# Kernel optimization log

Hardware: AMD Instinct MI355X
Metric: run time of the kernel (lower is better)

Reference implementation:

```python
import jax, jax.numpy as jnp
import numpy as np

B, F, D = 16384, 256, 128
H = [512, 256]
OUT = 8
VOCAB = 100000


def setup_inputs() -> dict:
    key = jax.random.key(0)
    ks = jax.random.split(key, 16)
    s = lambda k, *sh: jax.random.normal(k, sh, jnp.float32) * 0.05
    return dict(
        features=jax.random.normal(ks[0], (B, F), jnp.float32),
        ent_idx=jax.random.randint(ks[1], (B,), 0, VOCAB),
        target=jax.random.randint(ks[2], (B,), 0, OUT),
        Wf=s(ks[3], F, D), bf=jnp.zeros((D,), jnp.float32),
        Wu=s(ks[4], D, D), bu=jnp.zeros((D,), jnp.float32),
        w_cf=s(ks[5], D), w_fc=s(ks[6], D),
        w_ef=s(ks[7], D), w_fe=s(ks[8], D),
        b_c=jnp.zeros((1,), jnp.float32), b_e=jnp.zeros((1,), jnp.float32),
        head_tab=s(ks[9], VOCAB, D), ent_tab=s(ks[10], VOCAB, D),
        W0=s(ks[11], 2 * D, H[0]), b0=jnp.zeros((H[0],), jnp.float32),
        W1=s(ks[12], H[0], H[1]), b1=jnp.zeros((H[1],), jnp.float32),
        W2=s(ks[13], H[1], OUT), b2=jnp.zeros((OUT,), jnp.float32),
    )


def cross_compress(f, e, w_cf, w_fc, w_ef, w_fe, b_c, b_e):
    # torch code builds c = f (outer) e of shape (B,D,D) then matmuls a (D,1)
    # vector; algebraically (f e^T) w = f * (e . w), so we use the O(B*D) form.
    ew_cf = e @ w_cf  # (B,)
    fw_fc = f @ w_fc
    ew_ef = e @ w_ef
    fw_fe = f @ w_fe
    new_f = f * ew_cf[:, None] + e * fw_fc[:, None] + b_c
    new_e = f * ew_ef[:, None] + e * fw_fe[:, None] + b_e
    return new_f, new_e


def reference(features, ent_idx, target, Wf, bf, Wu, bu, w_cf, w_fc, w_ef,
              w_fe, b_c, b_e, head_tab, ent_tab, W0, b0, W1, b1, W2, b2):
    # 'rec' branch of CompanyOperationEvaluation.forward (eval mode, dropout=id)
    cf = jax.nn.relu(features @ Wf + bf)          # feature_layer
    e = ent_tab[ent_idx]                           # entity_embed lookup
    h = head_tab[ent_idx]                          # head_embed lookup (same ids)
    for _ in range(2):
        cf = jax.nn.relu(cf @ Wu + bu)             # user_low_mlp_layer
        h, e = cross_compress(h, e, w_cf, w_fc, w_ef, w_fe, b_c, b_e)
    high = jnp.concatenate([cf, e], axis=1)        # (B, 2D)
    x = jax.nn.relu(high @ W0 + b0)
    x = jax.nn.relu(x @ W1 + b1)
    x = jax.nn.relu(x @ W2 + b2)                   # pred_last_layer
    prob = jax.nn.softmax(x, axis=1)
    return (prob, target)
```

## Files before the change

kernel.cpp:

```cpp
#include <hip/hip_runtime.h>
#include <hip/hip_bf16.h>


typedef __bf16 bf16x8 __attribute__((ext_vector_type(8)));
typedef float floatx4 __attribute__((ext_vector_type(4)));

__device__ __forceinline__ unsigned short f2bf(float x) {
  unsigned int u = __builtin_bit_cast(unsigned int, x);
  u = (u + 0x7FFFu + ((u >> 16) & 1u)) >> 16;
  return (unsigned short)u;
}

__device__ __forceinline__ int sz(int row, int col) {
  return col ^ ((row & 7) << 3);
}

#define PHASE_BAR()                                                  \
  do {                                                               \
    asm volatile("s_waitcnt vmcnt(0) lgkmcnt(0)" ::: "memory");      \
    __builtin_amdgcn_s_barrier();                                    \
    __builtin_amdgcn_sched_barrier(0);                               \
  } while (0)

__global__ __launch_bounds__(256) void prep_kernel(
    const float* __restrict__ Wf, const float* __restrict__ Wu,
    const float* __restrict__ W0, const float* __restrict__ W1,
    const float* __restrict__ W2,
    unsigned short* __restrict__ wfT, unsigned short* __restrict__ wuT,
    unsigned short* __restrict__ w0T, unsigned short* __restrict__ w1T,
    unsigned short* __restrict__ w2T) {
  __shared__ unsigned short tile[32][34];
  const int bid = blockIdx.x, tid = threadIdx.x;
  if (bid < 304) {
    int t = bid;
    const float* src; unsigned short* dst; int N, K, kt, nt;
    if (t < 32)       { src = Wf; dst = wfT; N = 128; K = 256; kt = t >> 2;       nt = t & 3; }
    else if (t < 48)  { t -= 32;  src = Wu; dst = wuT; N = 128; K = 128; kt = t >> 2; nt = t & 3; }
    else if (t < 176) { t -= 48;  src = W0; dst = w0T; N = 512; K = 256; kt = t >> 4; nt = t & 15; }
    else              { t -= 176; src = W1; dst = w1T; N = 256; K = 512; kt = t >> 3; nt = t & 7; }
    {
      int r = tid >> 3, cg = (tid & 7) * 4;
      float4 v = *(const float4*)(src + (size_t)(kt * 32 + r) * N + nt * 32 + cg);
      tile[r][cg + 0] = f2bf(v.x); tile[r][cg + 1] = f2bf(v.y);
      tile[r][cg + 2] = f2bf(v.z); tile[r][cg + 3] = f2bf(v.w);
    }
    __syncthreads();
    {
      int rp = tid >> 3, cg = (tid & 7) * 4;
      uint2 o;
      o.x = (unsigned)tile[cg + 0][rp] | ((unsigned)tile[cg + 1][rp] << 16);
      o.y = (unsigned)tile[cg + 2][rp] | ((unsigned)tile[cg + 3][rp] << 16);
      *(uint2*)(dst + (size_t)(nt * 32 + rp) * K + kt * 32 + cg) = o;
    }
  } else {
#pragma unroll
    for (int i = 0; i < 8; ++i) {
      int g = tid * 8 + i, k = g >> 3, n = g & 7;
      w2T[n * 256 + k] = f2bf(W2[g]);
    }
  }
}

template <int LDK>
__device__ __forceinline__ void stageB(unsigned short* dstbase,
                                       const unsigned short* __restrict__ src,
                                       int tid) {
#pragma unroll
  for (int i = 0; i < 4; ++i) {
    int chunk = i * 256 + tid;
    int row = chunk >> 3, segs = chunk & 7;
    int segl = segs ^ (row & 7);
    const unsigned short* g = src + (size_t)row * LDK + segl * 8;
    unsigned short* d = dstbase + chunk * 8;
    __builtin_amdgcn_global_load_lds((const unsigned int*)g, (unsigned int*)d,
                                     16, 0, 0);
  }
}

template <int PASS_STEPS, int LDK>
__device__ __forceinline__ const unsigned short* srcstep(
    const unsigned short* __restrict__ s, int st) {
  return s + (size_t)(st / PASS_STEPS) * 128 * LDK + (st % PASS_STEPS) * 64;
}

template <int LDA>
__device__ __forceinline__ void mstep(const unsigned short* A,
                                      const unsigned short* bt, int k0,
                                      floatx4* acc, int m16, int quad,
                                      int wave) {
#pragma unroll
  for (int kk = 0; kk < 64; kk += 32) {
    const int ca = k0 + kk + quad * 8;
    const int cb = kk + quad * 8;
    const int ra0 = m16, ra1 = 16 + m16;
    const int rb0 = wave * 32 + m16, rb1 = wave * 32 + 16 + m16;
    bf16x8 a0 = *(const bf16x8*)&A[ra0 * LDA + sz(ra0, ca)];
    bf16x8 a1 = *(const bf16x8*)&A[ra1 * LDA + sz(ra1, ca)];
    bf16x8 b0 = *(const bf16x8*)&bt[rb0 * 64 + sz(rb0, cb)];
    bf16x8 b1 = *(const bf16x8*)&bt[rb1 * 64 + sz(rb1, cb)];
    acc[0] = __builtin_amdgcn_mfma_f32_16x16x32_bf16(a0, b0, acc[0], 0, 0, 0);
    acc[1] = __builtin_amdgcn_mfma_f32_16x16x32_bf16(a0, b1, acc[1], 0, 0, 0);
    acc[2] = __builtin_amdgcn_mfma_f32_16x16x32_bf16(a1, b0, acc[2], 0, 0, 0);
    acc[3] = __builtin_amdgcn_mfma_f32_16x16x32_bf16(a1, b1, acc[3], 0, 0, 0);
  }
}

template <int T, int LDA, int PASS_STEPS, int LDK>
__device__ __forceinline__ void gemm_phase(
    const unsigned short* A, const unsigned short* __restrict__ src,
    unsigned short* b_sh, floatx4* acc, int tid, int m16, int quad, int wave) {
  stageB<LDK>(b_sh, srcstep<PASS_STEPS, LDK>(src, 0), tid);
  PHASE_BAR();
#pragma unroll
  for (int t = 0; t < T; ++t) {
    if (t + 1 < T)
      stageB<LDK>(b_sh + ((t + 1) & 1) * 8192,
                  srcstep<PASS_STEPS, LDK>(src, t + 1), tid);
    mstep<LDA>(A, b_sh + (t & 1) * 8192, (t % PASS_STEPS) * 64,
               acc + (t / PASS_STEPS) * 4, m16, quad, wave);
    PHASE_BAR();
  }
}

__global__ __launch_bounds__(256, 2) void fused_mlp_kernel(
    const float* __restrict__ features, const int* __restrict__ ent_idx,
    const float* __restrict__ head_tab, const float* __restrict__ ent_tab,
    const float* __restrict__ w_cf, const float* __restrict__ w_fc,
    const float* __restrict__ w_ef, const float* __restrict__ w_fe,
    const float* __restrict__ b_c, const float* __restrict__ b_e,
    const unsigned short* __restrict__ wfT,
    const unsigned short* __restrict__ wuT, const float* __restrict__ bf_,
    const float* __restrict__ bu,
    const unsigned short* __restrict__ w0T, const float* __restrict__ b0,
    const unsigned short* __restrict__ w1T, const float* __restrict__ b1,
    const unsigned short* __restrict__ w2T, const float* __restrict__ b2,
    const int* __restrict__ target, float* __restrict__ out) {
  __shared__ __align__(16) unsigned short regionA[16384];
  __shared__ __align__(16) unsigned short b_sh[2 * 8192];
  __shared__ __align__(16) unsigned short w2_sh[2048];
  __shared__ __align__(16) float cw_sh[512];
  unsigned short* feat_sh = regionA;
  unsigned short* buf0 = regionA + 8192;
  unsigned short* buf1 = regionA + 12288;
  unsigned short* A_sh = regionA;
  unsigned short* x0_sh = regionA;
  unsigned short* x1_sh = b_sh;

  const int tid = threadIdx.x;
  const int r0 = blockIdx.x * 32;
  const int lane = tid & 63, wave = tid >> 6;
  const int m16 = lane & 15, quad = lane >> 4;

  const int grow = tid >> 3, gpart = tid & 7;
  const int gidx = ent_idx[r0 + grow];
  const float* hp = head_tab + (size_t)gidx * 128 + gpart * 16;
  const float* ep = ent_tab + (size_t)gidx * 128 + gpart * 16;
  float4 h4[4], e4[4];
#pragma unroll
  for (int j = 0; j < 4; ++j) {
    h4[j] = *(const float4*)(hp + j * 4);
    e4[j] = *(const float4*)(ep + j * 4);
  }
  if (tid < 128) {
    int a = tid >> 5, o = (tid & 31) * 4;
    const float* s = (a == 0) ? w_cf : (a == 1) ? w_fc : (a == 2) ? w_ef : w_fe;
    *(float4*)&cw_sh[a * 128 + o] = *(const float4*)(s + o);
  }
  *(uint4*)&w2_sh[tid * 8] = *(const uint4*)(w2T + tid * 8);

#pragma unroll
  for (int i = 0; i < 8; ++i) {
    int idx4 = i * 256 + tid;
    int row = idx4 >> 6, c = (idx4 & 63) * 4;
    float4 v = *(const float4*)(features + (size_t)(r0 + row) * 256 + c);
    uint2 o;
    o.x = (unsigned)f2bf(v.x) | ((unsigned)f2bf(v.y) << 16);
    o.y = (unsigned)f2bf(v.z) | ((unsigned)f2bf(v.w) << 16);
    *(uint2*)&feat_sh[row * 256 + sz(row, c)] = o;
  }

  floatx4 acc[4];
#pragma unroll
  for (int j = 0; j < 4; ++j) acc[j] = (floatx4){0.f, 0.f, 0.f, 0.f};
  gemm_phase<4, 256, 4, 256>(feat_sh, wfT, b_sh, acc, tid, m16, quad, wave);
#pragma unroll
  for (int mi = 0; mi < 2; ++mi)
#pragma unroll
    for (int ni = 0; ni < 2; ++ni) {
      int col = wave * 32 + ni * 16 + m16;
      float bv = bf_[col];
#pragma unroll
      for (int r = 0; r < 4; ++r) {
        int row = mi * 16 + quad * 4 + r;
        buf0[row * 128 + sz(row, col)] =
            f2bf(fmaxf(acc[mi * 2 + ni][r] + bv, 0.f));
      }
    }

  {
    float h[16], e[16];
#pragma unroll
    for (int j = 0; j < 4; ++j) {
      h[4 * j + 0] = h4[j].x; h[4 * j + 1] = h4[j].y;
      h[4 * j + 2] = h4[j].z; h[4 * j + 3] = h4[j].w;
      e[4 * j + 0] = e4[j].x; e[4 * j + 1] = e4[j].y;
      e[4 * j + 2] = e4[j].z; e[4 * j + 3] = e4[j].w;
    }
    const float bc = b_c[0], be = b_e[0];
#pragma unroll
    for (int it = 0; it < 2; ++it) {
      float d0 = 0.f, d1 = 0.f, d2 = 0.f, d3 = 0.f;
#pragma unroll
      for (int j = 0; j < 16; ++j) {
        float wcf = cw_sh[0 * 128 + gpart * 16 + j];
        float wfc = cw_sh[1 * 128 + gpart * 16 + j];
        float wef = cw_sh[2 * 128 + gpart * 16 + j];
        float wfe = cw_sh[3 * 128 + gpart * 16 + j];
        d0 += e[j] * wcf; d1 += h[j] * wfc;
        d2 += e[j] * wef; d3 += h[j] * wfe;
      }
#pragma unroll
      for (int s = 1; s < 8; s <<= 1) {
        d0 += __shfl_xor(d0, s); d1 += __shfl_xor(d1, s);
        d2 += __shfl_xor(d2, s); d3 += __shfl_xor(d3, s);
      }
#pragma unroll
      for (int j = 0; j < 16; ++j) {
        float nh = h[j] * d0 + e[j] * d1 + bc;
        float ne = h[j] * d2 + e[j] * d3 + be;
        h[j] = nh; e[j] = ne;
      }
    }
    uint4 o0, o1;
    unsigned* w = (unsigned*)&o0;
#pragma unroll
    for (int j = 0; j < 4; ++j)
      w[j] = (unsigned)f2bf(e[2 * j]) | ((unsigned)f2bf(e[2 * j + 1]) << 16);
    w = (unsigned*)&o1;
#pragma unroll
    for (int j = 0; j < 4; ++j)
      w[j] = (unsigned)f2bf(e[8 + 2 * j]) |
             ((unsigned)f2bf(e[8 + 2 * j + 1]) << 16);
    const int c0 = 128 + gpart * 16;
    *(uint4*)&A_sh[grow * 256 + sz(grow, c0)] = o0;
    *(uint4*)&A_sh[grow * 256 + sz(grow, c0 + 8)] = o1;
  }

#pragma unroll
  for (int j = 0; j < 4; ++j) acc[j] = (floatx4){0.f, 0.f, 0.f, 0.f};
  gemm_phase<2, 128, 2, 128>(buf0, wuT, b_sh, acc, tid, m16, quad, wave);
#pragma unroll
  for (int mi = 0; mi < 2; ++mi)
#pragma unroll
    for (int ni = 0; ni < 2; ++ni) {
      int col = wave * 32 + ni * 16 + m16;
      float bv = bu[col];
#pragma unroll
      for (int r = 0; r < 4; ++r) {
        int row = mi * 16 + quad * 4 + r;
        buf1[row * 128 + sz(row, col)] =
            f2bf(fmaxf(acc[mi * 2 + ni][r] + bv, 0.f));
      }
    }

#pragma unroll
  for (int j = 0; j < 4; ++j) acc[j] = (floatx4){0.f, 0.f, 0.f, 0.f};
  PHASE_BAR();
  mstep<128>(buf1, b_sh, 0, acc, m16, quad, wave);
  mstep<128>(buf1, b_sh + 8192, 64, acc, m16, quad, wave);
  PHASE_BAR();
#pragma unroll
  for (int mi = 0; mi < 2; ++mi)
#pragma unroll
    for (int ni = 0; ni < 2; ++ni) {
      int col = wave * 32 + ni * 16 + m16;
      float bv = bu[col];
#pragma unroll
      for (int r = 0; r < 4; ++r) {
        int row = mi * 16 + quad * 4 + r;
        A_sh[row * 256 + sz(row, col)] =
            f2bf(fmaxf(acc[mi * 2 + ni][r] + bv, 0.f));
      }
    }

  floatx4 acc16[16];
#pragma unroll
  for (int j = 0; j < 16; ++j) acc16[j] = (floatx4){0.f, 0.f, 0.f, 0.f};
  gemm_phase<16, 256, 4, 256>(A_sh, w0T, b_sh, acc16, tid, m16, quad, wave);
#pragma unroll
  for (int np = 0; np < 4; ++np)
#pragma unroll
    for (int mi = 0; mi < 2; ++mi)
#pragma unroll
      for (int ni = 0; ni < 2; ++ni) {
        int col = np * 128 + wave * 32 + ni * 16 + m16;
        float bv = b0[col];
#pragma unroll
        for (int r = 0; r < 4; ++r) {
          int row = mi * 16 + quad * 4 + r;
          x0_sh[row * 512 + sz(row, col)] =
              f2bf(fmaxf(acc16[np * 4 + mi * 2 + ni][r] + bv, 0.f));
        }
      }

  floatx4 acc8[8];
#pragma unroll
  for (int j = 0; j < 8; ++j) acc8[j] = (floatx4){0.f, 0.f, 0.f, 0.f};
  gemm_phase<16, 512, 8, 512>(x0_sh, w1T, b_sh, acc8, tid, m16, quad, wave);
#pragma unroll
  for (int np = 0; np < 2; ++np)
#pragma unroll
    for (int mi = 0; mi < 2; ++mi)
#pragma unroll
      for (int ni = 0; ni < 2; ++ni) {
        int col = np * 128 + wave * 32 + ni * 16 + m16;
        float bv = b1[col];
#pragma unroll
        for (int r = 0; r < 4; ++r)
          x1_sh[(mi * 16 + quad * 4 + r) * 264 + col] =
              f2bf(fmaxf(acc8[np * 4 + mi * 2 + ni][r] + bv, 0.f));
      }
  PHASE_BAR();

  {
    int row = tid >> 3, q = tid & 7;
    float p[8];
#pragma unroll
    for (int n = 0; n < 8; ++n) p[n] = 0.f;
#pragma unroll
    for (int jb = 0; jb < 4; ++jb) {
      bf16x8 xv = *(const bf16x8*)&x1_sh[row * 264 + q * 32 + jb * 8];
#pragma unroll
      for (int n = 0; n < 8; ++n) {
        bf16x8 wv = *(const bf16x8*)&w2_sh[n * 256 + q * 32 + jb * 8];
#pragma unroll
        for (int j = 0; j < 8; ++j) p[n] += (float)xv[j] * (float)wv[j];
      }
    }
#pragma unroll
    for (int s = 1; s < 8; s <<= 1)
#pragma unroll
      for (int n = 0; n < 8; ++n) p[n] += __shfl_xor(p[n], s);
    if (q == 0) {
      float mx = -1e30f;
#pragma unroll
      for (int n = 0; n < 8; ++n) {
        p[n] = fmaxf(p[n] + b2[n], 0.f);
        mx = fmaxf(mx, p[n]);
      }
      float sum = 0.f;
#pragma unroll
      for (int n = 0; n < 8; ++n) { p[n] = __expf(p[n] - mx); sum += p[n]; }
      const float inv = 1.f / sum;
      const int gr = r0 + row;
      float4 o0 = {p[0] * inv, p[1] * inv, p[2] * inv, p[3] * inv};
      float4 o1 = {p[4] * inv, p[5] * inv, p[6] * inv, p[7] * inv};
      *(float4*)(out + (size_t)gr * 8) = o0;
      *(float4*)(out + (size_t)gr * 8 + 4) = o1;
      out[16384 * 8 + gr] = (float)target[gr];
    }
  }
}

extern "C" void kernel_launch(void* const* d_in, const int* in_sizes, int n_in,
                              void* d_out, int out_size, void* d_ws, size_t ws_size,
                              hipStream_t stream) {
  const float* features = (const float*)d_in[0];
  const int* ent_idx    = (const int*)d_in[1];
  const int* target     = (const int*)d_in[2];
  const float* Wf  = (const float*)d_in[3];
  const float* bf_ = (const float*)d_in[4];
  const float* Wu  = (const float*)d_in[5];
  const float* bu  = (const float*)d_in[6];
  const float* w_cf = (const float*)d_in[7];
  const float* w_fc = (const float*)d_in[8];
  const float* w_ef = (const float*)d_in[9];
  const float* w_fe = (const float*)d_in[10];
  const float* b_c  = (const float*)d_in[11];
  const float* b_e  = (const float*)d_in[12];
  const float* head_tab = (const float*)d_in[13];
  const float* ent_tab  = (const float*)d_in[14];
  const float* W0 = (const float*)d_in[15];
  const float* b0 = (const float*)d_in[16];
  const float* W1 = (const float*)d_in[17];
  const float* b1 = (const float*)d_in[18];
  const float* W2 = (const float*)d_in[19];
  const float* b2 = (const float*)d_in[20];
  float* out = (float*)d_out;

  unsigned short* ws = (unsigned short*)d_ws;
  size_t off = 0;
  auto alloc = [&](size_t n) { unsigned short* p = ws + off; off += n; return p; };
  unsigned short* wfT  = alloc(32768);
  unsigned short* wuT  = alloc(16384);
  unsigned short* w0T  = alloc(131072);
  unsigned short* w1T  = alloc(131072);
  unsigned short* w2T  = alloc(2048);
  (void)ws_size; (void)in_sizes; (void)n_in; (void)out_size;

  prep_kernel<<<305, 256, 0, stream>>>(Wf, Wu, W0, W1, W2,
                                       wfT, wuT, w0T, w1T, w2T);
  fused_mlp_kernel<<<512, 256, 0, stream>>>(features, ent_idx, head_tab,
      ent_tab, w_cf, w_fc, w_ef, w_fe, b_c, b_e, wfT, wuT, bf_, bu,
      w0T, b0, w1T, b1, w2T, b2, target, out);
}
```

Baseline: 185.2 us.

## Triple-buffer weight staging with partial vmcnt waits in fused MLP

Weight-tile staging in the GEMM phases moves from double to triple buffering: two tiles are prefetched ahead and barriers wait only until a few loads remain outstanding (vmcnt(4)) rather than draining all global loads. The goal is to overlap global loads with MFMA work better. To make room in LDS, the cross-compress weight vectors are aliased into an unused activation buffer and the small W2 shared copy is dropped, so the final layer reads W2 straight from global memory. The partial-wait count is tied to how many loads stageB issues per thread, and the larger LDS footprint may reduce occupancy below two blocks per CU.

```diff
diff --git a/kernel.cpp b/kernel.cpp
--- a/kernel.cpp
+++ b/kernel.cpp
@@ -15,11 +15,11 @@
   return col ^ ((row & 7) << 3);
 }
 
-#define PHASE_BAR()                                                  \
-  do {                                                               \
-    asm volatile("s_waitcnt vmcnt(0) lgkmcnt(0)" ::: "memory");      \
-    __builtin_amdgcn_s_barrier();                                    \
-    __builtin_amdgcn_sched_barrier(0);                               \
+#define BAR_VM(N)                                                      \
+  do {                                                                 \
+    asm volatile("s_waitcnt vmcnt(" #N ") lgkmcnt(0)" ::: "memory");   \
+    __builtin_amdgcn_s_barrier();                                      \
+    __builtin_amdgcn_sched_barrier(0);                                 \
   } while (0)
 
 __global__ __launch_bounds__(256) void prep_kernel(
@@ -110,15 +110,24 @@
     const unsigned short* A, const unsigned short* __restrict__ src,
     unsigned short* b_sh, floatx4* acc, int tid, int m16, int quad, int wave) {
   stageB<LDK>(b_sh, srcstep<PASS_STEPS, LDK>(src, 0), tid);
-  PHASE_BAR();
+  if (T > 1) {
+    stageB<LDK>(b_sh + 8192, srcstep<PASS_STEPS, LDK>(src, 1), tid);
+    BAR_VM(4);
+  } else {
+    BAR_VM(0);
+  }
 #pragma unroll
   for (int t = 0; t < T; ++t) {
-    if (t + 1 < T)
-      stageB<LDK>(b_sh + ((t + 1) & 1) * 8192,
-                  srcstep<PASS_STEPS, LDK>(src, t + 1), tid);
-    mstep<LDA>(A, b_sh + (t & 1) * 8192, (t % PASS_STEPS) * 64,
+    if (t + 2 < T)
+      stageB<LDK>(b_sh + ((t + 2) % 3) * 8192,
+                  srcstep<PASS_STEPS, LDK>(src, t + 2), tid);
+    mstep<LDA>(A, b_sh + (t % 3) * 8192, (t % PASS_STEPS) * 64,
                acc + (t / PASS_STEPS) * 4, m16, quad, wave);
-    PHASE_BAR();
+    if (t + 2 < T) {
+      BAR_VM(4);
+    } else {
+      BAR_VM(0);
+    }
   }
 }
 
@@ -136,15 +145,14 @@
     const unsigned short* __restrict__ w2T, const float* __restrict__ b2,
     const int* __restrict__ target, float* __restrict__ out) {
   __shared__ __align__(16) unsigned short regionA[16384];
-  __shared__ __align__(16) unsigned short b_sh[2 * 8192];
-  __shared__ __align__(16) unsigned short w2_sh[2048];
-  __shared__ __align__(16) float cw_sh[512];
+  __shared__ __align__(16) unsigned short b_sh[3 * 8192];
   unsigned short* feat_sh = regionA;
   unsigned short* buf0 = regionA + 8192;
   unsigned short* buf1 = regionA + 12288;
   unsigned short* A_sh = regionA;
   unsigned short* x0_sh = regionA;
   unsigned short* x1_sh = b_sh;
+  float* cw_p = (float*)buf1;
 
   const int tid = threadIdx.x;
   const int r0 = blockIdx.x * 32;
@@ -164,9 +172,8 @@
   if (tid < 128) {
     int a = tid >> 5, o = (tid & 31) * 4;
     const float* s = (a == 0) ? w_cf : (a == 1) ? w_fc : (a == 2) ? w_ef : w_fe;
-    *(float4*)&cw_sh[a * 128 + o] = *(const float4*)(s + o);
-  }
-  *(uint4*)&w2_sh[tid * 8] = *(const uint4*)(w2T + tid * 8);
+    *(float4*)&cw_p[a * 128 + o] = *(const float4*)(s + o);
+  }
 
 #pragma unroll
   for (int i = 0; i < 8; ++i) {
@@ -212,10 +219,10 @@
       float d0 = 0.f, d1 = 0.f, d2 = 0.f, d3 = 0.f;
 #pragma unroll
       for (int j = 0; j < 16; ++j) {
-        float wcf = cw_sh[0 * 128 + gpart * 16 + j];
-        float wfc = cw_sh[1 * 128 + gpart * 16 + j];
-        float wef = cw_sh[2 * 128 + gpart * 16 + j];
-        float wfe = cw_sh[3 * 128 + gpart * 16 + j];
+        float wcf = cw_p[0 * 128 + gpart * 16 + j];
+        float wfc = cw_p[1 * 128 + gpart * 16 + j];
+        float wef = cw_p[2 * 128 + gpart * 16 + j];
+        float wfe = cw_p[3 * 128 + gpart * 16 + j];
         d0 += e[j] * wcf; d1 += h[j] * wfc;
         d2 += e[j] * wef; d3 += h[j] * wfe;
       }
@@ -265,10 +272,10 @@
 
 #pragma unroll
   for (int j = 0; j < 4; ++j) acc[j] = (floatx4){0.f, 0.f, 0.f, 0.f};
-  PHASE_BAR();
+  BAR_VM(0);
   mstep<128>(buf1, b_sh, 0, acc, m16, quad, wave);
   mstep<128>(buf1, b_sh + 8192, 64, acc, m16, quad, wave);
-  PHASE_BAR();
+  BAR_VM(0);
 #pragma unroll
   for (int mi = 0; mi < 2; ++mi)
 #pragma unroll
@@ -320,7 +327,7 @@
           x1_sh[(mi * 16 + quad * 4 + r) * 264 + col] =
               f2bf(fmaxf(acc8[np * 4 + mi * 2 + ni][r] + bv, 0.f));
       }
-  PHASE_BAR();
+  BAR_VM(0);
 
   {
     int row = tid >> 3, q = tid & 7;
@@ -332,7 +339,7 @@
       bf16x8 xv = *(const bf16x8*)&x1_sh[row * 264 + q * 32 + jb * 8];
 #pragma unroll
       for (int n = 0; n < 8; ++n) {
-        bf16x8 wv = *(const bf16x8*)&w2_sh[n * 256 + q * 32 + jb * 8];
+        bf16x8 wv = *(const bf16x8*)(w2T + n * 256 + q * 32 + jb * 8);
 #pragma unroll
         for (int j = 0; j < 8; ++j) p[n] += (float)xv[j] * (float)wv[j];
       }
```

New measurement: 181.7 us. About the same (-1.9%).
